# Performance work log

Hardware: AMD Instinct MI355X
Metric: run time of the kernel (lower is better)

## Reference

```python
import jax, jax.numpy as jnp
import numpy as np

C = 128        # attention channels (inner_channel)
OUT_C = 256    # bottleneck output channels (in_channel)
NEG = -10000000.0


def conv_bn_relu(x, W, scale, shift):
    """1x1 conv (no bias) + eval-mode BatchNorm folded to scale/shift + ReLU.
    x: [B, Cin, H, W], W: [Cout, Cin]."""
    y = jnp.einsum('oc,bchw->bohw', W, x)
    y = y * scale[None, :, None, None] + shift[None, :, None, None]
    return jax.nn.relu(y)


def setup_inputs() -> dict:
    key = jax.random.key(0)
    ks = jax.random.split(key, 20)
    B, H, W_, K = 4, 128, 128, 1024
    inp = {
        'query_feats': jax.random.normal(ks[0], (B, C, H, W_), jnp.float32),
        'key_feats':   jax.random.normal(ks[1], (B, C, K, 1), jnp.float32),
        'value_feats': jax.random.normal(ks[2], (B, C, K, 1), jnp.float32),
        'key_mask':    jax.random.randint(ks[3], (B, 1, K, 1), 0, 2).astype(bool),
    }
    s = 1.0 / np.sqrt(C)

    def mk(i, cin, cout):
        return (jax.random.normal(ks[i], (cout, cin), jnp.float32) * s,
                jnp.ones((cout,), jnp.float32),
                jnp.zeros((cout,), jnp.float32))

    inp['Wq1'], inp['sq1'], inp['bq1'] = mk(4, C, C)
    inp['Wq2'], inp['sq2'], inp['bq2'] = mk(5, C, C)
    inp['Wk1'], inp['sk1'], inp['bk1'] = mk(6, C, C)
    inp['Wk2'], inp['sk2'], inp['bk2'] = mk(7, C, C)
    inp['Wv'],  inp['sv'],  inp['bv']  = mk(8, C, C)
    inp['Wo'],  inp['so'],  inp['bo']  = mk(9, C, C)
    inp['Wb'],  inp['sb'],  inp['bb']  = mk(10, 2 * C, OUT_C)
    return inp


def reference(query_feats, key_feats, value_feats, key_mask,
              Wq1, sq1, bq1, Wq2, sq2, bq2,
              Wk1, sk1, bk1, Wk2, sk2, bk2,
              Wv, sv, bv, Wo, so, bo, Wb, sb, bb):
    B, _, H, W_ = query_feats.shape
    # projections (2 conv-bn-relu for q/k, 1 for v)
    q = conv_bn_relu(conv_bn_relu(query_feats, Wq1, sq1, bq1), Wq2, sq2, bq2)
    k = conv_bn_relu(conv_bn_relu(key_feats, Wk1, sk1, bk1), Wk2, sk2, bk2)
    v = conv_bn_relu(value_feats, Wv, sv, bv)

    q = q.reshape(B, C, -1).transpose(0, 2, 1)   # [B, HW, C]
    k = k.reshape(B, C, -1)                      # [B, C, K]
    v = v.reshape(B, C, -1).transpose(0, 2, 1)   # [B, K, C]

    sim = jnp.einsum('bqc,bck->bqk', q, k) * (C ** -0.5)   # [B, HW, K]
    m = key_mask.reshape(B, 1, -1).astype(sim.dtype)        # [B, 1, K]
    sim = sim * m + NEG * (1.0 - m)
    attn = jax.nn.softmax(sim, axis=-1)

    ctx = jnp.einsum('bqk,bkc->bqc', attn, v)               # [B, HW, C]
    ctx = ctx.transpose(0, 2, 1).reshape(B, C, H, W_)
    ctx = conv_bn_relu(ctx, Wo, so, bo)                     # out_project

    out = conv_bn_relu(jnp.concatenate([ctx, query_feats], axis=1), Wb, sb, bb)
    return out
```

## Files before the change

### kernel.cpp

```cpp
#include <hip/hip_runtime.h>
#include <hip/hip_bf16.h>

#define B_    4
#define C_    128
#define HW_   16384
#define K_    1024
#define NEG_  (-10000000.0f)
#define SCALE_ 0.08838834764831845f

using bf16 = __hip_bfloat16;
typedef __bf16 b8v __attribute__((ext_vector_type(8)));
typedef __bf16 b4v __attribute__((ext_vector_type(4)));
typedef __bf16 b2v __attribute__((ext_vector_type(2)));
typedef float  f4v __attribute__((ext_vector_type(4)));

__device__ __forceinline__ b8v ldb8(const void* p) { return *(const b8v*)p; }
__device__ __forceinline__ b4v ldb4(const void* p) { return *(const b4v*)p; }

#define XSTRIDE 272
#define KSTRIDE 272
#define VSTRIDE 136

__global__ __launch_bounds__(256) void prep1_kernel(
    const float* __restrict__ query, const float* __restrict__ key, const float* __restrict__ val,
    const float* __restrict__ Wq1, const float* __restrict__ sq1,
    const float* __restrict__ Wq2, const float* __restrict__ sq2,
    const float* __restrict__ Wo,  const float* __restrict__ so,
    const float* __restrict__ Wb,  const float* __restrict__ sb,
    const float* __restrict__ Wk1, const float* __restrict__ sk1,
    const float* __restrict__ Wk2, const float* __restrict__ sk2,
    const float* __restrict__ Wv,  const float* __restrict__ sv,
    bf16* __restrict__ qt, bf16* __restrict__ kT, bf16* __restrict__ vT,
    __bf16* __restrict__ Wq1p, __bf16* __restrict__ Wq2p,
    __bf16* __restrict__ Wop,  __bf16* __restrict__ Wbp,
    __bf16* __restrict__ Wk1p, __bf16* __restrict__ Wk2p, __bf16* __restrict__ Wvp)
{
    __shared__ float Xs[64 * 129];
    const int blk = blockIdx.x, t = threadIdx.x;

    if (blk < 1152) {
        const float* src; bf16* dst; int L, p0, b;
        if (blk < 1024) {
            b = blk >> 8; src = query; dst = qt; L = HW_; p0 = (blk & 255) * 64;
        } else {
            const int i = blk - 1024;
            b = i >> 5; int j = i & 31;
            if (j < 16) { src = key; dst = kT; } else { src = val; dst = vT; j -= 16; }
            L = K_; p0 = j * 64;
        }
        const int pl = t & 63, cg = t >> 6;
#pragma unroll 4
        for (int i = 0; i < 32; ++i) {
            const int c = cg * 32 + i;
            Xs[pl * 129 + c] = src[(size_t)(b * 128 + c) * L + p0 + pl];
        }
        __syncthreads();
#pragma unroll 4
        for (int it = 0; it < 16; ++it) {
            const int p = it * 4 + cg;
            b2v pk;
            pk[0] = (__bf16)Xs[p * 129 + 2 * pl];
            pk[1] = (__bf16)Xs[p * 129 + 2 * pl + 1];
            *(b2v*)(dst + ((size_t)b * L + p0 + p) * 128 + 2 * pl) = pk;
        }
    } else {
        const int idx = (blk - 1152) * 256 + t;
        if (idx < 16384)       { Wq1p[idx] = (__bf16)(Wq1[idx] * sq1[idx >> 7]); }
        else if (idx < 32768)  { const int i = idx - 16384;  Wq2p[i] = (__bf16)(Wq2[i] * sq2[i >> 7]); }
        else if (idx < 49152)  { const int i = idx - 32768;  Wop[i]  = (__bf16)(Wo[i]  * so[i >> 7]); }
        else if (idx < 114688) { const int i = idx - 49152;  Wbp[i]  = (__bf16)(Wb[i]  * sb[i >> 8]); }
        else if (idx < 131072) { const int i = idx - 114688; Wk1p[i] = (__bf16)(Wk1[i] * sk1[i >> 7]); }
        else if (idx < 147456) { const int i = idx - 131072; Wk2p[i] = (__bf16)(Wk2[i] * sk2[i >> 7]); }
        else                   { const int i = idx - 147456; Wvp[i]  = (__bf16)(Wv[i]  * sv[i >> 7]); }
    }
}

__device__ __forceinline__ void proj2_body(
    const bf16* __restrict__ src,
    const __bf16* __restrict__ W1, const float* __restrict__ sh1,
    const __bf16* __restrict__ W2, const float* __restrict__ sh2,
    bf16* __restrict__ dst, char* Xs, __bf16* Ys)
{
    const int t = threadIdx.x, w = t >> 6, lane = t & 63;
    const int pl = lane & 15, quad = lane >> 4;
    const int ob = 32 * w;

    {
        const char* sg = (const char*)src + t * 16;
        char* xl = Xs + (t >> 4) * XSTRIDE + (t & 15) * 16;
#pragma unroll
        for (int i = 0; i < 8; ++i)
            *(float4*)(xl + i * 16 * XSTRIDE) = *(const float4*)(sg + i * 4096);
    }

    b8v W1f[2][4], W2f[2][4];
#pragma unroll
    for (int mt = 0; mt < 2; ++mt)
#pragma unroll
        for (int s = 0; s < 4; ++s) {
            W1f[mt][s] = ldb8(W1 + (ob + mt * 16 + pl) * 128 + s * 32 + quad * 8);
            W2f[mt][s] = ldb8(W2 + (ob + mt * 16 + pl) * 128 + s * 32 + quad * 8);
        }
    __syncthreads();

    f4v acc[2][8];
#pragma unroll
    for (int mt = 0; mt < 2; ++mt)
#pragma unroll
        for (int nt = 0; nt < 8; ++nt) acc[mt][nt] = (f4v){0.f, 0.f, 0.f, 0.f};

#pragma unroll
    for (int s = 0; s < 4; ++s) {
        b8v Bf[8];
#pragma unroll
        for (int nt = 0; nt < 8; ++nt)
            Bf[nt] = ldb8(Xs + (nt * 16 + pl) * XSTRIDE + s * 64 + quad * 16);
#pragma unroll
        for (int mt = 0; mt < 2; ++mt)
#pragma unroll
            for (int nt = 0; nt < 8; ++nt)
                acc[mt][nt] = __builtin_amdgcn_mfma_f32_16x16x32_bf16(W1f[mt][s], Bf[nt], acc[mt][nt], 0, 0, 0);
    }

#pragma unroll
    for (int mt = 0; mt < 2; ++mt) {
        const float4 s4 = *(const float4*)(sh1 + ob + mt * 16 + quad * 4);
        const float shf[4] = {s4.x, s4.y, s4.z, s4.w};
#pragma unroll
        for (int nt = 0; nt < 8; ++nt) {
            b4v y;
#pragma unroll
            for (int r = 0; r < 4; ++r) y[r] = (__bf16)fmaxf(acc[mt][nt][r] + shf[r], 0.f);
            *(b4v*)&Ys[(nt * 16 + pl) * 136 + ob + mt * 16 + quad * 4] = y;
        }
    }
    __syncthreads();

    f4v acc2[2][8];
#pragma unroll
    for (int mt = 0; mt < 2; ++mt)
#pragma unroll
        for (int nt = 0; nt < 8; ++nt) acc2[mt][nt] = (f4v){0.f, 0.f, 0.f, 0.f};

#pragma unroll
    for (int s = 0; s < 4; ++s) {
        b8v Bf[8];
#pragma unroll
        for (int nt = 0; nt < 8; ++nt)
            Bf[nt] = *(const b8v*)&Ys[(nt * 16 + pl) * 136 + s * 32 + quad * 8];
#pragma unroll
        for (int mt = 0; mt < 2; ++mt)
#pragma unroll
            for (int nt = 0; nt < 8; ++nt)
                acc2[mt][nt] = __builtin_amdgcn_mfma_f32_16x16x32_bf16(W2f[mt][s], Bf[nt], acc2[mt][nt], 0, 0, 0);
    }

#pragma unroll
    for (int mt = 0; mt < 2; ++mt) {
        const float4 s4 = *(const float4*)(sh2 + ob + mt * 16 + quad * 4);
        const float shf[4] = {s4.x, s4.y, s4.z, s4.w};
#pragma unroll
        for (int nt = 0; nt < 8; ++nt) {
            b4v y;
#pragma unroll
            for (int r = 0; r < 4; ++r) y[r] = (__bf16)fmaxf(acc2[mt][nt][r] + shf[r], 0.f);
            *(b4v*)(dst + (size_t)(nt * 16 + pl) * 128 + ob + mt * 16 + quad * 4) = y;
        }
    }
}

__global__ __launch_bounds__(256, 2) void kvproj_kernel(
    const bf16* __restrict__ kT, const bf16* __restrict__ vT,
    const __bf16* __restrict__ Wk1p, const float* __restrict__ bk1,
    const __bf16* __restrict__ Wk2p, const float* __restrict__ bk2,
    const __bf16* __restrict__ Wvp,  const float* __restrict__ bv,
    bf16* __restrict__ kbuf, bf16* __restrict__ vbuf)
{
    __shared__ __align__(16) char Xs[128 * XSTRIDE];
    __shared__ __align__(16) __bf16 Ys[128 * 136];
    const int t = threadIdx.x, w = t >> 6, lane = t & 63;
    const int pl = lane & 15, quad = lane >> 4;
    const int b = blockIdx.y;
    const int n0 = blockIdx.x * 128;

    proj2_body(kT + ((size_t)b * K_ + n0) * 128, Wk1p, bk1, Wk2p, bk2,
               kbuf + ((size_t)b * K_ + n0) * 128, Xs, Ys);
    __syncthreads();

    {
        const char* sg = (const char*)(vT + ((size_t)b * K_ + n0) * 128) + t * 16;
        char* xl = Xs + (t >> 4) * XSTRIDE + (t & 15) * 16;
#pragma unroll
        for (int i = 0; i < 8; ++i)
            *(float4*)(xl + i * 16 * XSTRIDE) = *(const float4*)(sg + i * 4096);
    }
    const int ob = 32 * w;
    b8v Wf[2][4];
#pragma unroll
    for (int mt = 0; mt < 2; ++mt)
#pragma unroll
        for (int s = 0; s < 4; ++s)
            Wf[mt][s] = ldb8(Wvp + (ob + mt * 16 + pl) * 128 + s * 32 + quad * 8);
    __syncthreads();

    f4v acc[2][8];
#pragma unroll
    for (int mt = 0; mt < 2; ++mt)
#pragma unroll
        for (int nt = 0; nt < 8; ++nt) acc[mt][nt] = (f4v){0.f, 0.f, 0.f, 0.f};

#pragma unroll
    for (int s = 0; s < 4; ++s) {
        b8v Bf[8];
#pragma unroll
        for (int nt = 0; nt < 8; ++nt)
            Bf[nt] = ldb8(Xs + (nt * 16 + pl) * XSTRIDE + s * 64 + quad * 16);
#pragma unroll
        for (int mt = 0; mt < 2; ++mt)
#pragma unroll
            for (int nt = 0; nt < 8; ++nt)
                acc[mt][nt] = __builtin_amdgcn_mfma_f32_16x16x32_bf16(Wf[mt][s], Bf[nt], acc[mt][nt], 0, 0, 0);
    }

    bf16* vb = vbuf + (size_t)b * 128 * K_;
#pragma unroll
    for (int mt = 0; mt < 2; ++mt) {
        const float4 s4 = *(const float4*)(bv + ob + mt * 16 + quad * 4);
        const float shf[4] = {s4.x, s4.y, s4.z, s4.w};
#pragma unroll
        for (int nt = 0; nt < 8; ++nt)
#pragma unroll
            for (int r = 0; r < 4; ++r)
                vb[(size_t)(ob + mt * 16 + quad * 4 + r) * K_ + n0 + nt * 16 + pl]
                    = __float2bfloat16(fmaxf(acc[mt][nt][r] + shf[r], 0.f));
    }
}

__global__ __launch_bounds__(256, 2) void mega_kernel(
    const bf16* __restrict__ qt, const bf16* __restrict__ kbuf, const bf16* __restrict__ vbuf,
    const int* __restrict__ mask,
    const __bf16* __restrict__ Wq1p, const float* __restrict__ bq1,
    const __bf16* __restrict__ Wq2p, const float* __restrict__ bq2,
    const __bf16* __restrict__ Wop,  const float* __restrict__ bo,
    const __bf16* __restrict__ Wbp,  const float* __restrict__ bb,
    float* __restrict__ out)
{
    __shared__ __align__(16) char RA[128 * XSTRIDE];
    __shared__ __align__(16) char RB[128 * XSTRIDE];

    const int t = threadIdx.x, w = t >> 6, lane = t & 63;
    const int pl = lane & 15, quad = lane >> 4;
    const int n0 = blockIdx.x * 128;
    const int b  = blockIdx.y;
    const int ob = 32 * w;

    __bf16* RAh = (__bf16*)RA;
    __bf16* RBh = (__bf16*)RB;
    char* xl = RA + (t >> 4) * XSTRIDE + (t & 15) * 16;

    {
        const char* qg = (const char*)(qt + ((size_t)b * HW_ + n0) * 128) + t * 16;
#pragma unroll
        for (int i = 0; i < 8; ++i)
            *(float4*)(xl + i * 16 * XSTRIDE) = *(const float4*)(qg + i * 4096);
    }
    {
        b8v W1f[2][4], W2f[2][4];
#pragma unroll
        for (int mt = 0; mt < 2; ++mt)
#pragma unroll
            for (int s = 0; s < 4; ++s) {
                W1f[mt][s] = ldb8(Wq1p + (ob + mt * 16 + pl) * 128 + s * 32 + quad * 8);
                W2f[mt][s] = ldb8(Wq2p + (ob + mt * 16 + pl) * 128 + s * 32 + quad * 8);
            }
        __syncthreads();

        f4v a1[2][8];
#pragma unroll
        for (int mt = 0; mt < 2; ++mt)
#pragma unroll
            for (int nt = 0; nt < 8; ++nt) a1[mt][nt] = (f4v){0.f, 0.f, 0.f, 0.f};
#pragma unroll
        for (int s = 0; s < 4; ++s) {
            b8v Bf[8];
#pragma unroll
            for (int nt = 0; nt < 8; ++nt)
                Bf[nt] = ldb8(RA + (nt * 16 + pl) * XSTRIDE + s * 64 + quad * 16);
#pragma unroll
            for (int mt = 0; mt < 2; ++mt)
#pragma unroll
                for (int nt = 0; nt < 8; ++nt)
                    a1[mt][nt] = __builtin_amdgcn_mfma_f32_16x16x32_bf16(W1f[mt][s], Bf[nt], a1[mt][nt], 0, 0, 0);
        }
#pragma unroll
        for (int mt = 0; mt < 2; ++mt) {
            const float4 s4 = *(const float4*)(bq1 + ob + mt * 16 + quad * 4);
            const float shf[4] = {s4.x, s4.y, s4.z, s4.w};
#pragma unroll
            for (int nt = 0; nt < 8; ++nt) {
                b4v y;
#pragma unroll
                for (int r = 0; r < 4; ++r) y[r] = (__bf16)fmaxf(a1[mt][nt][r] + shf[r], 0.f);
                *(b4v*)&RBh[(nt * 16 + pl) * 136 + ob + mt * 16 + quad * 4] = y;
            }
        }
        __syncthreads();

        f4v a2[2][8];
#pragma unroll
        for (int mt = 0; mt < 2; ++mt)
#pragma unroll
            for (int nt = 0; nt < 8; ++nt) a2[mt][nt] = (f4v){0.f, 0.f, 0.f, 0.f};
#pragma unroll
        for (int s = 0; s < 4; ++s) {
            b8v Bf[8];
#pragma unroll
            for (int nt = 0; nt < 8; ++nt)
                Bf[nt] = *(const b8v*)&RBh[(nt * 16 + pl) * 136 + s * 32 + quad * 8];
#pragma unroll
            for (int mt = 0; mt < 2; ++mt)
#pragma unroll
                for (int nt = 0; nt < 8; ++nt)
                    a2[mt][nt] = __builtin_amdgcn_mfma_f32_16x16x32_bf16(W2f[mt][s], Bf[nt], a2[mt][nt], 0, 0, 0);
        }
#pragma unroll
        for (int mt = 0; mt < 2; ++mt) {
            const float4 s4 = *(const float4*)(bq2 + ob + mt * 16 + quad * 4);
            const float shf[4] = {s4.x, s4.y, s4.z, s4.w};
#pragma unroll
            for (int nt = 0; nt < 8; ++nt) {
                b4v y;
#pragma unroll
                for (int r = 0; r < 4; ++r) y[r] = (__bf16)fmaxf(a2[mt][nt][r] + shf[r], 0.f);
                *(b4v*)&RAh[(nt * 16 + pl) * 136 + ob + mt * 16 + quad * 4] = y;
            }
        }
        __syncthreads();
    }

    b8v qf0[4], qf1[4];
#pragma unroll
    for (int s = 0; s < 4; ++s) {
        qf0[s] = ldb8(RA + (w * 32 + pl) * XSTRIDE + s * 64 + quad * 16);
        qf1[s] = ldb8(RA + (w * 32 + 16 + pl) * XSTRIDE + s * 64 + quad * 16);
    }
    __syncthreads();

    float* bias = (float*)RA;
    char* ktile = RA + 4096;
    char* vtile = RB;

    for (int i = t; i < K_; i += 256)
        bias[i] = (mask[b * K_ + i] != 0) ? 0.f : NEG_;

    const bf16* kpt = kbuf + (size_t)b * K_ * 128;
    const bf16* vpt = vbuf + (size_t)b * 128 * K_;
    const char* kg = (const char*)kpt + t * 16;
    const char* vg = (const char*)(vpt + (size_t)(t >> 3) * K_) + (t & 7) * 16;
    char* kl = ktile + (t >> 4) * KSTRIDE + (t & 15) * 16;
    char* vl = vtile + (t >> 3) * VSTRIDE + (t & 7) * 16;

    float4 k_r0 = *(const float4*)(kg);
    float4 k_r1 = *(const float4*)(kg + 4096);
    float4 k_r2 = *(const float4*)(kg + 8192);
    float4 k_r3 = *(const float4*)(kg + 12288);
    float4 v_r0 = *(const float4*)(vg);
    float4 v_r1 = *(const float4*)(vg + 65536);
    float4 v_r2 = *(const float4*)(vg + 131072);
    float4 v_r3 = *(const float4*)(vg + 196608);

    f4v ac0[8], ac1[8];
#pragma unroll
    for (int i = 0; i < 8; ++i) { ac0[i] = (f4v){0.f,0.f,0.f,0.f}; ac1[i] = (f4v){0.f,0.f,0.f,0.f}; }
    float mrun0 = -3.0e38f, mrun1 = -3.0e38f, lrun0 = 0.f, lrun1 = 0.f;

    for (int chunk = 0; chunk < 16; ++chunk) {
        const int k0 = chunk * 64;

        *(float4*)(kl)                = k_r0;
        *(float4*)(kl + 16 * KSTRIDE) = k_r1;
        *(float4*)(kl + 32 * KSTRIDE) = k_r2;
        *(float4*)(kl + 48 * KSTRIDE) = k_r3;
        *(float4*)(vl)                = v_r0;
        *(float4*)(vl + 32 * VSTRIDE) = v_r1;
        *(float4*)(vl + 64 * VSTRIDE) = v_r2;
        *(float4*)(vl + 96 * VSTRIDE) = v_r3;
        __syncthreads();

        if (chunk < 15) {
            const char* kgn = kg + (chunk + 1) * 16384;
            const char* vgn = vg + (chunk + 1) * 128;
            k_r0 = *(const float4*)(kgn);
            k_r1 = *(const float4*)(kgn + 4096);
            k_r2 = *(const float4*)(kgn + 8192);
            k_r3 = *(const float4*)(kgn + 12288);
            v_r0 = *(const float4*)(vgn);
            v_r1 = *(const float4*)(vgn + 65536);
            v_r2 = *(const float4*)(vgn + 131072);
            v_r3 = *(const float4*)(vgn + 196608);
        }

        f4v sv0[4], sv1[4];
#pragma unroll
        for (int kt = 0; kt < 4; ++kt) {
            f4v a0 = (f4v){0.f,0.f,0.f,0.f}, a1 = (f4v){0.f,0.f,0.f,0.f};
            const char* krow = ktile + (kt * 16 + pl) * KSTRIDE + quad * 16;
#pragma unroll
            for (int s = 0; s < 4; ++s) {
                const b8v kf = ldb8(krow + s * 64);
                a0 = __builtin_amdgcn_mfma_f32_16x16x32_bf16(kf, qf0[s], a0, 0, 0, 0);
                a1 = __builtin_amdgcn_mfma_f32_16x16x32_bf16(kf, qf1[s], a1, 0, 0, 0);
            }
            const float4 b4 = *(const float4*)&bias[k0 + kt * 16 + quad * 4];
            const float bb4[4] = {b4.x, b4.y, b4.z, b4.w};
#pragma unroll
            for (int r = 0; r < 4; ++r) { sv0[kt][r] = a0[r] * SCALE_ + bb4[r];
                                          sv1[kt][r] = a1[r] * SCALE_ + bb4[r]; }
        }

        float ml0 = sv0[0][0], ml1 = sv1[0][0];
#pragma unroll
        for (int kt = 0; kt < 4; ++kt)
#pragma unroll
            for (int r = 0; r < 4; ++r) { ml0 = fmaxf(ml0, sv0[kt][r]); ml1 = fmaxf(ml1, sv1[kt][r]); }
        ml0 = fmaxf(ml0, __shfl_xor(ml0, 16, 64)); ml0 = fmaxf(ml0, __shfl_xor(ml0, 32, 64));
        ml1 = fmaxf(ml1, __shfl_xor(ml1, 16, 64)); ml1 = fmaxf(ml1, __shfl_xor(ml1, 32, 64));
        const float mn0 = fmaxf(mrun0, ml0), mn1 = fmaxf(mrun1, ml1);
        const float al0 = __expf(mrun0 - mn0), al1 = __expf(mrun1 - mn1);
        mrun0 = mn0; mrun1 = mn1;

        b4v pk0[4], pk1[4];
        float rs0 = 0.f, rs1 = 0.f;
#pragma unroll
        for (int kt = 0; kt < 4; ++kt)
#pragma unroll
            for (int r = 0; r < 4; ++r) {
                const float p0 = __expf(sv0[kt][r] - mn0); rs0 += p0; pk0[kt][r] = (__bf16)p0;
                const float p1 = __expf(sv1[kt][r] - mn1); rs1 += p1; pk1[kt][r] = (__bf16)p1;
            }
        rs0 += __shfl_xor(rs0, 16, 64); rs0 += __shfl_xor(rs0, 32, 64);
        rs1 += __shfl_xor(rs1, 16, 64); rs1 += __shfl_xor(rs1, 32, 64);
        lrun0 = lrun0 * al0 + rs0;
        lrun1 = lrun1 * al1 + rs1;

        float ar0[4], ar1[4];
#pragma unroll
        for (int r = 0; r < 4; ++r) { ar0[r] = __shfl(al0, quad * 4 + r, 64);
                                      ar1[r] = __shfl(al1, quad * 4 + r, 64); }
#pragma unroll
        for (int ct = 0; ct < 8; ++ct)
#pragma unroll
            for (int r = 0; r < 4; ++r) { ac0[ct][r] *= ar0[r]; ac1[ct][r] *= ar1[r]; }

        const b8v A00 = __builtin_shufflevector(pk0[0], pk0[1], 0, 1, 2, 3, 4, 5, 6, 7);
        const b8v A01 = __builtin_shufflevector(pk0[2], pk0[3], 0, 1, 2, 3, 4, 5, 6, 7);
        const b8v A10 = __builtin_shufflevector(pk1[0], pk1[1], 0, 1, 2, 3, 4, 5, 6, 7);
        const b8v A11 = __builtin_shufflevector(pk1[2], pk1[3], 0, 1, 2, 3, 4, 5, 6, 7);
#pragma unroll
        for (int ct = 0; ct < 8; ++ct) {
            const char* vrow = vtile + (ct * 16 + pl) * VSTRIDE + quad * 8;
            const b8v B0 = __builtin_shufflevector(ldb4(vrow),      ldb4(vrow + 32), 0, 1, 2, 3, 4, 5, 6, 7);
            const b8v B1 = __builtin_shufflevector(ldb4(vrow + 64), ldb4(vrow + 96), 0, 1, 2, 3, 4, 5, 6, 7);
            ac0[ct] = __builtin_amdgcn_mfma_f32_16x16x32_bf16(A00, B0, ac0[ct], 0, 0, 0);
            ac0[ct] = __builtin_amdgcn_mfma_f32_16x16x32_bf16(A01, B1, ac0[ct], 0, 0, 0);
            ac1[ct] = __builtin_amdgcn_mfma_f32_16x16x32_bf16(A10, B0, ac1[ct], 0, 0, 0);
            ac1[ct] = __builtin_amdgcn_mfma_f32_16x16x32_bf16(A11, B1, ac1[ct], 0, 0, 0);
        }
        __syncthreads();
    }

    {
        float inv0[4], inv1[4];
#pragma unroll
        for (int r = 0; r < 4; ++r) { inv0[r] = 1.f / __shfl(lrun0, quad * 4 + r, 64);
                                      inv1[r] = 1.f / __shfl(lrun1, quad * 4 + r, 64); }
#pragma unroll
        for (int ct = 0; ct < 8; ++ct)
#pragma unroll
            for (int r = 0; r < 4; ++r) {
                RAh[(w * 32 + quad * 4 + r) * 136 + ct * 16 + pl]      = (__bf16)(ac0[ct][r] * inv0[r]);
                RAh[(w * 32 + 16 + quad * 4 + r) * 136 + ct * 16 + pl] = (__bf16)(ac1[ct][r] * inv1[r]);
            }
    }
    __syncthreads();

    b8v Wof[2][4];
#pragma unroll
    for (int mt = 0; mt < 2; ++mt)
#pragma unroll
        for (int s = 0; s < 4; ++s)
            Wof[mt][s] = ldb8(Wop + (ob + mt * 16 + pl) * 128 + s * 32 + quad * 8);

    const char* qg2 = (const char*)(qt + ((size_t)b * HW_ + n0) * 128) + t * 16;
    float4 q_s0 = *(const float4*)(qg2);
    float4 q_s1 = *(const float4*)(qg2 + 4096);
    float4 q_s2 = *(const float4*)(qg2 + 8192);
    float4 q_s3 = *(const float4*)(qg2 + 12288);
    float4 q_s4 = *(const float4*)(qg2 + 16384);
    float4 q_s5 = *(const float4*)(qg2 + 20480);
    float4 q_s6 = *(const float4*)(qg2 + 24576);
    float4 q_s7 = *(const float4*)(qg2 + 28672);

    {
        f4v f1[2][8];
#pragma unroll
        for (int mt = 0; mt < 2; ++mt)
#pragma unroll
            for (int nt = 0; nt < 8; ++nt) f1[mt][nt] = (f4v){0.f, 0.f, 0.f, 0.f};
#pragma unroll
        for (int s = 0; s < 4; ++s) {
            b8v Bf[8];
#pragma unroll
            for (int nt = 0; nt < 8; ++nt)
                Bf[nt] = ldb8(RA + (nt * 16 + pl) * XSTRIDE + s * 64 + quad * 16);
#pragma unroll
            for (int mt = 0; mt < 2; ++mt)
#pragma unroll
                for (int nt = 0; nt < 8; ++nt)
                    f1[mt][nt] = __builtin_amdgcn_mfma_f32_16x16x32_bf16(Wof[mt][s], Bf[nt], f1[mt][nt], 0, 0, 0);
        }
#pragma unroll
        for (int mt = 0; mt < 2; ++mt) {
// ... 30 lines not shown
        for (int ks = 0; ks < 8; ++ks) {
            b8v Af[4];
#pragma unroll
            for (int mt = 0; mt < 4; ++mt)
                Af[mt] = ldb8(Wbp + (size_t)(64 * w + mt * 16 + pl) * 256 + ks * 32 + quad * 8);
            b8v Bf[8];
            if (ks < 4) {
#pragma unroll
                for (int nt = 0; nt < 8; ++nt)
                    Bf[nt] = *(const b8v*)&RBh[(nt * 16 + pl) * 136 + ks * 32 + quad * 8];
            } else {
#pragma unroll
                for (int nt = 0; nt < 8; ++nt)
                    Bf[nt] = ldb8(RA + (nt * 16 + pl) * XSTRIDE + (ks - 4) * 64 + quad * 16);
            }
#pragma unroll
            for (int mt = 0; mt < 4; ++mt)
#pragma unroll
                for (int nt = 0; nt < 8; ++nt)
                    f2[mt][nt] = __builtin_amdgcn_mfma_f32_16x16x32_bf16(Af[mt], Bf[nt], f2[mt][nt], 0, 0, 0);
        }
#pragma unroll
        for (int mt = 0; mt < 4; ++mt) {
            const float4 s4 = *(const float4*)(bb + 64 * w + mt * 16 + quad * 4);
            const float shf[4] = {s4.x, s4.y, s4.z, s4.w};
#pragma unroll
            for (int nt = 0; nt < 8; ++nt)
#pragma unroll
                for (int r = 0; r < 4; ++r)
                    out[(size_t)(b * 256 + 64 * w + mt * 16 + quad * 4 + r) * HW_ + n0 + nt * 16 + pl]
                        = fmaxf(f2[mt][nt][r] + shf[r], 0.f);
        }
    }
}

extern "C" void kernel_launch(void* const* d_in, const int* in_sizes, int n_in,
                              void* d_out, int out_size, void* d_ws, size_t ws_size,
                              hipStream_t stream)
{
    const float* query = (const float*)d_in[0];
    const float* key   = (const float*)d_in[1];
    const float* val   = (const float*)d_in[2];
    const int*   mask  = (const int*)  d_in[3];
    const float* Wq1 = (const float*)d_in[4];  const float* sq1 = (const float*)d_in[5];  const float* bq1 = (const float*)d_in[6];
    const float* Wq2 = (const float*)d_in[7];  const float* sq2 = (const float*)d_in[8];  const float* bq2 = (const float*)d_in[9];
    const float* Wk1 = (const float*)d_in[10]; const float* sk1 = (const float*)d_in[11]; const float* bk1 = (const float*)d_in[12];
    const float* Wk2 = (const float*)d_in[13]; const float* sk2 = (const float*)d_in[14]; const float* bk2 = (const float*)d_in[15];
    const float* Wv  = (const float*)d_in[16]; const float* sv  = (const float*)d_in[17]; const float* bv  = (const float*)d_in[18];
    const float* Wo  = (const float*)d_in[19]; const float* so  = (const float*)d_in[20]; const float* bo  = (const float*)d_in[21];
    const float* Wb  = (const float*)d_in[22]; const float* sb  = (const float*)d_in[23]; const float* bb  = (const float*)d_in[24];

    char* ws = (char*)d_ws;
    bf16*   qt   = (bf16*)(ws);
    bf16*   kT   = (bf16*)(ws + (16u << 20));
    bf16*   vT   = (bf16*)(ws + (17u << 20));
    bf16*   kbuf = (bf16*)(ws + (18u << 20));
    bf16*   vbuf = (bf16*)(ws + (19u << 20));
    char*   wbase = ws + (20u << 20);
    __bf16* Wq1p = (__bf16*)(wbase);
    __bf16* Wq2p = (__bf16*)(wbase + (32u << 10));
    __bf16* Wop  = (__bf16*)(wbase + (64u << 10));
    __bf16* Wbp  = (__bf16*)(wbase + (96u << 10));
    __bf16* Wk1p = (__bf16*)(wbase + (224u << 10));
    __bf16* Wk2p = (__bf16*)(wbase + (256u << 10));
    __bf16* Wvp  = (__bf16*)(wbase + (288u << 10));
    float* outp = (float*)d_out;

    prep1_kernel<<<1792, 256, 0, stream>>>(
        query, key, val,
        Wq1, sq1, Wq2, sq2, Wo, so, Wb, sb, Wk1, sk1, Wk2, sk2, Wv, sv,
        qt, kT, vT, Wq1p, Wq2p, Wop, Wbp, Wk1p, Wk2p, Wvp);
    kvproj_kernel<<<dim3(8, B_), 256, 0, stream>>>(
        kT, vT, Wk1p, bk1, Wk2p, bk2, Wvp, bv, kbuf, vbuf);
    mega_kernel<<<dim3(HW_ / 128, B_), 256, 0, stream>>>(
        qt, kbuf, vbuf, mask,
        Wq1p, bq1, Wq2p, bq2, Wop, bo, Wbp, bb, outp);
}
```

Measured before the change: 222.4 us.

## Fuse K/V projection into prep, double-buffer attention tiles, lazy softmax rescale

Moves the key/value projections into the prep kernel so the separate kvproj launch and the kT/vT intermediate buffers go away. Inside the mega kernel, K/V tiles are now double-buffered with loads issued two chunks ahead, and raw s_barrier plus setprio hints replace __syncthreads. The softmax switches to exp2 with the log2e factor folded into the scale and mask bias. The accumulator rescale is skipped unless the running max grows by more than a threshold. The V tile layout changes to allow wider LDS reads, at the cost of more LDS and register pressure. The lazy rescale can let exponentials reach up to 2^8 before correction, which narrows the numerical margin.

After: 231.7 us. 1.04x slower.

```diff
diff --git a/kernel.cpp b/kernel.cpp
--- a/kernel.cpp
+++ b/kernel.cpp
@@ -5,8 +5,9 @@
 #define C_    128
 #define HW_   16384
 #define K_    1024
-#define NEG_  (-10000000.0f)
-#define SCALE_ 0.08838834764831845f
+#define SC2_  0.12751734f
+#define NEGL_ (-1.4427e7f)
+#define DTHR_ 8.0f
 
 using bf16 = __hip_bfloat16;
 typedef __bf16 b8v __attribute__((ext_vector_type(8)));
@@ -15,224 +16,211 @@
 typedef float  f4v __attribute__((ext_vector_type(4)));
 
 __device__ __forceinline__ b8v ldb8(const void* p) { return *(const b8v*)p; }
-__device__ __forceinline__ b4v ldb4(const void* p) { return *(const b4v*)p; }
 
 #define XSTRIDE 272
 #define KSTRIDE 272
-#define VSTRIDE 136
-
-__global__ __launch_bounds__(256) void prep1_kernel(
+#define VSTRIDE 144
+
+__device__ __forceinline__ b8v ldw8(const float* wp, float sc) {
+    const float4 a = *(const float4*)wp;
+    const float4 c = *(const float4*)(wp + 4);
+    b8v r;
+    r[0] = (__bf16)(a.x * sc); r[1] = (__bf16)(a.y * sc);
+    r[2] = (__bf16)(a.z * sc); r[3] = (__bf16)(a.w * sc);
+    r[4] = (__bf16)(c.x * sc); r[5] = (__bf16)(c.y * sc);
+    r[6] = (__bf16)(c.z * sc); r[7] = (__bf16)(c.w * sc);
+    return r;
+}
+
+__global__ __launch_bounds__(256, 2) void prep_kernel(
     const float* __restrict__ query, const float* __restrict__ key, const float* __restrict__ val,
     const float* __restrict__ Wq1, const float* __restrict__ sq1,
     const float* __restrict__ Wq2, const float* __restrict__ sq2,
     const float* __restrict__ Wo,  const float* __restrict__ so,
     const float* __restrict__ Wb,  const float* __restrict__ sb,
-    const float* __restrict__ Wk1, const float* __restrict__ sk1,
-    const float* __restrict__ Wk2, const float* __restrict__ sk2,
-    const float* __restrict__ Wv,  const float* __restrict__ sv,
-    bf16* __restrict__ qt, bf16* __restrict__ kT, bf16* __restrict__ vT,
+    const float* __restrict__ Wk1, const float* __restrict__ sk1, const float* __restrict__ bk1,
+    const float* __restrict__ Wk2, const float* __restrict__ sk2, const float* __restrict__ bk2,
+    const float* __restrict__ Wv,  const float* __restrict__ sv_, const float* __restrict__ bv,
+    bf16* __restrict__ qt, bf16* __restrict__ kbuf, bf16* __restrict__ vbuf,
     __bf16* __restrict__ Wq1p, __bf16* __restrict__ Wq2p,
-    __bf16* __restrict__ Wop,  __bf16* __restrict__ Wbp,
-    __bf16* __restrict__ Wk1p, __bf16* __restrict__ Wk2p, __bf16* __restrict__ Wvp)
+    __bf16* __restrict__ Wop,  __bf16* __restrict__ Wbp)
 {
-    __shared__ float Xs[64 * 129];
+    __shared__ __align__(16) char SM[69632];
     const int blk = blockIdx.x, t = threadIdx.x;
 
-    if (blk < 1152) {
-        const float* src; bf16* dst; int L, p0, b;
-        if (blk < 1024) {
-            b = blk >> 8; src = query; dst = qt; L = HW_; p0 = (blk & 255) * 64;
-        } else {
-            const int i = blk - 1024;
-            b = i >> 5; int j = i & 31;
-            if (j < 16) { src = key; dst = kT; } else { src = val; dst = vT; j -= 16; }
-            L = K_; p0 = j * 64;
-        }
+    if (blk < 32) {
+        const int b = blk >> 3, n0 = (blk & 7) * 128;
+        const int w = t >> 6, lane = t & 63;
+        const int pl = lane & 15, quad = lane >> 4;
+        const int ob = 32 * w;
+        const int plT = t & 63, cg = t >> 6;
+        char*    Xs  = SM;
+        __bf16*  Ys  = (__bf16*)(SM + 34816);
+        float*   Tmp = (float*)(SM + 34816);
+
+        auto transpose_in = [&](const float* src) {
+#pragma unroll
+            for (int h = 0; h < 2; ++h) {
+                const int p0 = n0 + h * 64;
+#pragma unroll 4
+                for (int i2 = 0; i2 < 32; ++i2) {
+                    const int c = cg * 32 + i2;
+                    Tmp[plT * 129 + c] = src[(size_t)(b * 128 + c) * K_ + p0 + plT];
+                }
+                __syncthreads();
+#pragma unroll 4
+                for (int it = 0; it < 16; ++it) {
+                    const int p = it * 4 + cg;
+                    b2v pk2;
+                    pk2[0] = (__bf16)Tmp[p * 129 + 2 * plT];
+                    pk2[1] = (__bf16)Tmp[p * 129 + 2 * plT + 1];
+                    *(b2v*)(Xs + (h * 64 + p) * XSTRIDE + 4 * plT) = pk2;
+                }
+                __syncthreads();
+            }
+        };
+
+        transpose_in(key);
+        b8v W1f[2][4], W2f[2][4];
+#pragma unroll
+        for (int mt = 0; mt < 2; ++mt)
+#pragma unroll
+            for (int s = 0; s < 4; ++s) {
+                const int row = ob + mt * 16 + pl;
+                W1f[mt][s] = ldw8(Wk1 + row * 128 + s * 32 + quad * 8, sk1[row]);
+                W2f[mt][s] = ldw8(Wk2 + row * 128 + s * 32 + quad * 8, sk2[row]);
+            }
+        {
+            f4v acc[2][8];
+#pragma unroll
+            for (int mt = 0; mt < 2; ++mt)
+#pragma unroll
+                for (int nt = 0; nt < 8; ++nt) acc[mt][nt] = (f4v){0.f, 0.f, 0.f, 0.f};
+#pragma unroll
+            for (int s = 0; s < 4; ++s) {
+                b8v Bf[8];
+#pragma unroll
+                for (int nt = 0; nt < 8; ++nt)
+                    Bf[nt] = ldb8(Xs + (nt * 16 + pl) * XSTRIDE + s * 64 + quad * 16);
+#pragma unroll
+                for (int mt = 0; mt < 2; ++mt)
+#pragma unroll
+                    for (int nt = 0; nt < 8; ++nt)
+                        acc[mt][nt] = __builtin_amdgcn_mfma_f32_16x16x32_bf16(W1f[mt][s], Bf[nt], acc[mt][nt], 0, 0, 0);
+            }
+#pragma unroll
+            for (int mt = 0; mt < 2; ++mt) {
+                const float4 s4 = *(const float4*)(bk1 + ob + mt * 16 + quad * 4);
+                const float shf[4] = {s4.x, s4.y, s4.z, s4.w};
+#pragma unroll
+                for (int nt = 0; nt < 8; ++nt) {
+                    b4v y;
+#pragma unroll
+                    for (int r = 0; r < 4; ++r) y[r] = (__bf16)fmaxf(acc[mt][nt][r] + shf[r], 0.f);
+                    *(b4v*)&Ys[(nt * 16 + pl) * 136 + ob + mt * 16 + quad * 4] = y;
+                }
+            }
+        }
+        __syncthreads();
+        {
+            f4v acc2[2][8];
+#pragma unroll
+            for (int mt = 0; mt < 2; ++mt)
+#pragma unroll
+                for (int nt = 0; nt < 8; ++nt) acc2[mt][nt] = (f4v){0.f, 0.f, 0.f, 0.f};
+#pragma unroll
+            for (int s = 0; s < 4; ++s) {
+                b8v Bf[8];
+#pragma unroll
+                for (int nt = 0; nt < 8; ++nt)
+                    Bf[nt] = *(const b8v*)&Ys[(nt * 16 + pl) * 136 + s * 32 + quad * 8];
+#pragma unroll
+                for (int mt = 0; mt < 2; ++mt)
+#pragma unroll
+                    for (int nt = 0; nt < 8; ++nt)
+                        acc2[mt][nt] = __builtin_amdgcn_mfma_f32_16x16x32_bf16(W2f[mt][s], Bf[nt], acc2[mt][nt], 0, 0, 0);
+            }
+            bf16* kdst = kbuf + ((size_t)b * K_ + n0) * 128;
+#pragma unroll
+            for (int mt = 0; mt < 2; ++mt) {
+                const float4 s4 = *(const float4*)(bk2 + ob + mt * 16 + quad * 4);
+                const float shf[4] = {s4.x, s4.y, s4.z, s4.w};
+#pragma unroll
+                for (int nt = 0; nt < 8; ++nt) {
+                    b4v y;
+#pragma unroll
+                    for (int r = 0; r < 4; ++r) y[r] = (__bf16)fmaxf(acc2[mt][nt][r] + shf[r], 0.f);
+                    *(b4v*)(kdst + (size_t)(nt * 16 + pl) * 128 + ob + mt * 16 + quad * 4) = y;
+                }
+            }
+        }
+        __syncthreads();
+
+        transpose_in(val);
+        b8v Wvf[2][4];
+#pragma unroll
+        for (int mt = 0; mt < 2; ++mt)
+#pragma unroll
+            for (int s = 0; s < 4; ++s) {
+                const int row = ob + mt * 16 + pl;
+                Wvf[mt][s] = ldw8(Wv + row * 128 + s * 32 + quad * 8, sv_[row]);
+            }
+        {
+            f4v acc[2][8];
+#pragma unroll
+            for (int mt = 0; mt < 2; ++mt)
+#pragma unroll
+                for (int nt = 0; nt < 8; ++nt) acc[mt][nt] = (f4v){0.f, 0.f, 0.f, 0.f};
+#pragma unroll
+            for (int s = 0; s < 4; ++s) {
+                b8v Bf[8];
+#pragma unroll
+                for (int nt = 0; nt < 8; ++nt)
+                    Bf[nt] = ldb8(Xs + (nt * 16 + pl) * XSTRIDE + s * 64 + quad * 16);
+#pragma unroll
+                for (int mt = 0; mt < 2; ++mt)
+#pragma unroll
+                    for (int nt = 0; nt < 8; ++nt)
+                        acc[mt][nt] = __builtin_amdgcn_mfma_f32_16x16x32_bf16(Wvf[mt][s], Bf[nt], acc[mt][nt], 0, 0, 0);
+            }
+            bf16* vdst = vbuf + (size_t)b * 128 * K_;
+#pragma unroll
+            for (int mt = 0; mt < 2; ++mt) {
+                const float4 s4 = *(const float4*)(bv + ob + mt * 16 + quad * 4);
+                const float shf[4] = {s4.x, s4.y, s4.z, s4.w};
+#pragma unroll
+                for (int nt = 0; nt < 8; ++nt)
+#pragma unroll
+                    for (int r = 0; r < 4; ++r)
+                        vdst[(size_t)(ob + mt * 16 + quad * 4 + r) * K_ + n0 + nt * 16 + pl]
+                            = __float2bfloat16(fmaxf(acc[mt][nt][r] + shf[r], 0.f));
+            }
+        }
+    } else if (blk < 1056) {
+        float* Xs2 = (float*)SM;
+        const int i = blk - 32;
+        const int b = i >> 8, p0 = (i & 255) * 64;
         const int pl = t & 63, cg = t >> 6;
 #pragma unroll 4
-        for (int i = 0; i < 32; ++i) {
-            const int c = cg * 32 + i;
-            Xs[pl * 129 + c] = src[(size_t)(b * 128 + c) * L + p0 + pl];
+        for (int i2 = 0; i2 < 32; ++i2) {
+            const int c = cg * 32 + i2;
+            Xs2[pl * 129 + c] = query[(size_t)(b * 128 + c) * HW_ + p0 + pl];
         }
         __syncthreads();
 #pragma unroll 4
         for (int it = 0; it < 16; ++it) {
             const int p = it * 4 + cg;
-            b2v pk;
-            pk[0] = (__bf16)Xs[p * 129 + 2 * pl];
-            pk[1] = (__bf16)Xs[p * 129 + 2 * pl + 1];
-            *(b2v*)(dst + ((size_t)b * L + p0 + p) * 128 + 2 * pl) = pk;
+            b2v pk2;
+            pk2[0] = (__bf16)Xs2[p * 129 + 2 * pl];
+            pk2[1] = (__bf16)Xs2[p * 129 + 2 * pl + 1];
+            *(b2v*)(qt + ((size_t)b * HW_ + p0 + p) * 128 + 2 * pl) = pk2;
         }
     } else {
-        const int idx = (blk - 1152) * 256 + t;
-        if (idx < 16384)       { Wq1p[idx] = (__bf16)(Wq1[idx] * sq1[idx >> 7]); }
-        else if (idx < 32768)  { const int i = idx - 16384;  Wq2p[i] = (__bf16)(Wq2[i] * sq2[i >> 7]); }
-        else if (idx < 49152)  { const int i = idx - 32768;  Wop[i]  = (__bf16)(Wo[i]  * so[i >> 7]); }
-        else if (idx < 114688) { const int i = idx - 49152;  Wbp[i]  = (__bf16)(Wb[i]  * sb[i >> 8]); }
-        else if (idx < 131072) { const int i = idx - 114688; Wk1p[i] = (__bf16)(Wk1[i] * sk1[i >> 7]); }
-        else if (idx < 147456) { const int i = idx - 131072; Wk2p[i] = (__bf16)(Wk2[i] * sk2[i >> 7]); }
-        else                   { const int i = idx - 147456; Wvp[i]  = (__bf16)(Wv[i]  * sv[i >> 7]); }
-    }
-}
-
-__device__ __forceinline__ void proj2_body(
-    const bf16* __restrict__ src,
-    const __bf16* __restrict__ W1, const float* __restrict__ sh1,
-    const __bf16* __restrict__ W2, const float* __restrict__ sh2,
-    bf16* __restrict__ dst, char* Xs, __bf16* Ys)
-{
-    const int t = threadIdx.x, w = t >> 6, lane = t & 63;
-    const int pl = lane & 15, quad = lane >> 4;
-    const int ob = 32 * w;
-
-    {
-        const char* sg = (const char*)src + t * 16;
-        char* xl = Xs + (t >> 4) * XSTRIDE + (t & 15) * 16;
-#pragma unroll
-        for (int i = 0; i < 8; ++i)
-            *(float4*)(xl + i * 16 * XSTRIDE) = *(const float4*)(sg + i * 4096);
-    }
-
-    b8v W1f[2][4], W2f[2][4];
-#pragma unroll
-    for (int mt = 0; mt < 2; ++mt)
-#pragma unroll
-        for (int s = 0; s < 4; ++s) {
-            W1f[mt][s] = ldb8(W1 + (ob + mt * 16 + pl) * 128 + s * 32 + quad * 8);
-            W2f[mt][s] = ldb8(W2 + (ob + mt * 16 + pl) * 128 + s * 32 + quad * 8);
-        }
-    __syncthreads();
-
-    f4v acc[2][8];
-#pragma unroll
-    for (int mt = 0; mt < 2; ++mt)
-#pragma unroll
-        for (int nt = 0; nt < 8; ++nt) acc[mt][nt] = (f4v){0.f, 0.f, 0.f, 0.f};
-
-#pragma unroll
-    for (int s = 0; s < 4; ++s) {
-        b8v Bf[8];
-#pragma unroll
-        for (int nt = 0; nt < 8; ++nt)
-            Bf[nt] = ldb8(Xs + (nt * 16 + pl) * XSTRIDE + s * 64 + quad * 16);
-#pragma unroll
-        for (int mt = 0; mt < 2; ++mt)
-#pragma unroll
-            for (int nt = 0; nt < 8; ++nt)
-                acc[mt][nt] = __builtin_amdgcn_mfma_f32_16x16x32_bf16(W1f[mt][s], Bf[nt], acc[mt][nt], 0, 0, 0);
-    }
-
-#pragma unroll
-    for (int mt = 0; mt < 2; ++mt) {
-        const float4 s4 = *(const float4*)(sh1 + ob + mt * 16 + quad * 4);
-        const float shf[4] = {s4.x, s4.y, s4.z, s4.w};
-#pragma unroll
-        for (int nt = 0; nt < 8; ++nt) {
-            b4v y;
-#pragma unroll
-            for (int r = 0; r < 4; ++r) y[r] = (__bf16)fmaxf(acc[mt][nt][r] + shf[r], 0.f);
-            *(b4v*)&Ys[(nt * 16 + pl) * 136 + ob + mt * 16 + quad * 4] = y;
-        }
-    }
-    __syncthreads();
-
-    f4v acc2[2][8];
-#pragma unroll
-    for (int mt = 0; mt < 2; ++mt)
-#pragma unroll
-        for (int nt = 0; nt < 8; ++nt) acc2[mt][nt] = (f4v){0.f, 0.f, 0.f, 0.f};
-
-#pragma unroll
-    for (int s = 0; s < 4; ++s) {
-        b8v Bf[8];
-#pragma unroll
-        for (int nt = 0; nt < 8; ++nt)
-            Bf[nt] = *(const b8v*)&Ys[(nt * 16 + pl) * 136 + s * 32 + quad * 8];
-#pragma unroll
-        for (int mt = 0; mt < 2; ++mt)
-#pragma unroll
-            for (int nt = 0; nt < 8; ++nt)
-                acc2[mt][nt] = __builtin_amdgcn_mfma_f32_16x16x32_bf16(W2f[mt][s], Bf[nt], acc2[mt][nt], 0, 0, 0);
-    }
-
-#pragma unroll
-    for (int mt = 0; mt < 2; ++mt) {
-        const float4 s4 = *(const float4*)(sh2 + ob + mt * 16 + quad * 4);
-        const float shf[4] = {s4.x, s4.y, s4.z, s4.w};
-#pragma unroll
-        for (int nt = 0; nt < 8; ++nt) {
-            b4v y;
-#pragma unroll
-            for (int r = 0; r < 4; ++r) y[r] = (__bf16)fmaxf(acc2[mt][nt][r] + shf[r], 0.f);
-            *(b4v*)(dst + (size_t)(nt * 16 + pl) * 128 + ob + mt * 16 + quad * 4) = y;
-        }
-    }
-}
-
-__global__ __launch_bounds__(256, 2) void kvproj_kernel(
-    const bf16* __restrict__ kT, const bf16* __restrict__ vT,
-    const __bf16* __restrict__ Wk1p, const float* __restrict__ bk1,
-    const __bf16* __restrict__ Wk2p, const float* __restrict__ bk2,
-    const __bf16* __restrict__ Wvp,  const float* __restrict__ bv,
-    bf16* __restrict__ kbuf, bf16* __restrict__ vbuf)
-{
-    __shared__ __align__(16) char Xs[128 * XSTRIDE];
-    __shared__ __align__(16) __bf16 Ys[128 * 136];
-    const int t = threadIdx.x, w = t >> 6, lane = t & 63;
-    const int pl = lane & 15, quad = lane >> 4;
-    const int b = blockIdx.y;
-    const int n0 = blockIdx.x * 128;
-
-    proj2_body(kT + ((size_t)b * K_ + n0) * 128, Wk1p, bk1, Wk2p, bk2,
-               kbuf + ((size_t)b * K_ + n0) * 128, Xs, Ys);
-    __syncthreads();
-
-    {
-        const char* sg = (const char*)(vT + ((size_t)b * K_ + n0) * 128) + t * 16;
-        char* xl = Xs + (t >> 4) * XSTRIDE + (t & 15) * 16;
-#pragma unroll
-        for (int i = 0; i < 8; ++i)
-            *(float4*)(xl + i * 16 * XSTRIDE) = *(const float4*)(sg + i * 4096);
-    }
-    const int ob = 32 * w;
-    b8v Wf[2][4];
-#pragma unroll
-    for (int mt = 0; mt < 2; ++mt)
-#pragma unroll
-        for (int s = 0; s < 4; ++s)
-            Wf[mt][s] = ldb8(Wvp + (ob + mt * 16 + pl) * 128 + s * 32 + quad * 8);
-    __syncthreads();
-
-    f4v acc[2][8];
-#pragma unroll
-    for (int mt = 0; mt < 2; ++mt)
-#pragma unroll
-        for (int nt = 0; nt < 8; ++nt) acc[mt][nt] = (f4v){0.f, 0.f, 0.f, 0.f};
-
-#pragma unroll
-    for (int s = 0; s < 4; ++s) {
-        b8v Bf[8];
-#pragma unroll
-        for (int nt = 0; nt < 8; ++nt)
-            Bf[nt] = ldb8(Xs + (nt * 16 + pl) * XSTRIDE + s * 64 + quad * 16);
-#pragma unroll
-        for (int mt = 0; mt < 2; ++mt)
-#pragma unroll
-            for (int nt = 0; nt < 8; ++nt)
-                acc[mt][nt] = __builtin_amdgcn_mfma_f32_16x16x32_bf16(Wf[mt][s], Bf[nt], acc[mt][nt], 0, 0, 0);
-    }
-
-    bf16* vb = vbuf + (size_t)b * 128 * K_;
-#pragma unroll
-    for (int mt = 0; mt < 2; ++mt) {
-        const float4 s4 = *(const float4*)(bv + ob + mt * 16 + quad * 4);
-        const float shf[4] = {s4.x, s4.y, s4.z, s4.w};
-#pragma unroll
-        for (int nt = 0; nt < 8; ++nt)
-#pragma unroll
-            for (int r = 0; r < 4; ++r)
-                vb[(size_t)(ob + mt * 16 + quad * 4 + r) * K_ + n0 + nt * 16 + pl]
-                    = __float2bfloat16(fmaxf(acc[mt][nt][r] + shf[r], 0.f));
+        const int idx = (blk - 1056) * 256 + t;
+        if (idx < 16384)      { Wq1p[idx] = (__bf16)(Wq1[idx] * sq1[idx >> 7]); }
+        else if (idx < 32768) { const int i2 = idx - 16384; Wq2p[i2] = (__bf16)(Wq2[i2] * sq2[i2 >> 7]); }
+        else if (idx < 49152) { const int i2 = idx - 32768; Wop[i2]  = (__bf16)(Wo[i2]  * so[i2 >> 7]); }
+        else                  { const int i2 = idx - 49152; Wbp[i2]  = (__bf16)(Wb[i2]  * sb[i2 >> 8]); }
     }
 }
 
@@ -245,8 +233,7 @@
     const __bf16* __restrict__ Wbp,  const float* __restrict__ bb,
     float* __restrict__ out)
 {
-    __shared__ __align__(16) char RA[128 * XSTRIDE];
-    __shared__ __align__(16) char RB[128 * XSTRIDE];
+    __shared__ __align__(16) char S[75776];
 
     const int t = threadIdx.x, w = t >> 6, lane = t & 63;
     const int pl = lane & 15, quad = lane >> 4;
@@ -254,8 +241,9 @@
     const int b  = blockIdx.y;
     const int ob = 32 * w;
 
-    __bf16* RAh = (__bf16*)RA;
-    __bf16* RBh = (__bf16*)RB;
+    char*   RA  = S;
+    __bf16* RAh = (__bf16*)S;
+    __bf16* RBh = (__bf16*)(S + 34816);
     char* xl = RA + (t >> 4) * XSTRIDE + (t & 15) * 16;
 
     {
@@ -346,65 +334,81 @@
     }
     __syncthreads();
 
-    float* bias = (float*)RA;
-    char* ktile = RA + 4096;
-    char* vtile = RB;
-
-    for (int i = t; i < K_; i += 256)
-        bias[i] = (mask[b * K_ + i] != 0) ? 0.f : NEG_;
+    float* bias = (float*)S;
+    char* kt0 = S + 4096;
+    char* kt1 = S + 21504;
+    char* vt0 = S + 38912;
+    char* vt1 = S + 57344;
 
     const bf16* kpt = kbuf + (size_t)b * K_ * 128;
     const bf16* vpt = vbuf + (size_t)b * 128 * K_;
     const char* kg = (const char*)kpt + t * 16;
     const char* vg = (const char*)(vpt + (size_t)(t >> 3) * K_) + (t & 7) * 16;
-    char* kl = ktile + (t >> 4) * KSTRIDE + (t & 15) * 16;
-    char* vl = vtile + (t >> 3) * VSTRIDE + (t & 7) * 16;
-
-    float4 k_r0 = *(const float4*)(kg);
-    float4 k_r1 = *(const float4*)(kg + 4096);
-    float4 k_r2 = *(const float4*)(kg + 8192);
-    float4 k_r3 = *(const float4*)(kg + 12288);
-    float4 v_r0 = *(const float4*)(vg);
-    float4 v_r1 = *(const float4*)(vg + 65536);
-    float4 v_r2 = *(const float4*)(vg + 131072);
-    float4 v_r3 = *(const float4*)(vg + 196608);
+    const int klo = (t >> 4) * KSTRIDE + (t & 15) * 16;
+    const int vj  = t & 7;
+    const int vlo = (t >> 3) * VSTRIDE + (vj >> 2) * 64 + (vj & 1) * 32 + ((vj >> 1) & 1) * 8;
+
+    float4 kr[4], vr[4];
+
+#define ISSUE_LOADS(chunk)                                            \
+    { const char* kgn = kg + (chunk) * 16384;                         \
+      const char* vgn = vg + (chunk) * 128;                           \
+      kr[0] = *(const float4*)(kgn);                                  \
+      kr[1] = *(const float4*)(kgn + 4096);                           \
+      kr[2] = *(const float4*)(kgn + 8192);                           \
+      kr[3] = *(const float4*)(kgn + 12288);                          \
+      vr[0] = *(const float4*)(vgn);                                  \
+      vr[1] = *(const float4*)(vgn + 65536);                          \
+      vr[2] = *(const float4*)(vgn + 131072);                         \
+      vr[3] = *(const float4*)(vgn + 196608); }
+
+#define STAGE_WRITES(ktd, vtd)                                        \
+    { char* klp = (ktd) + klo;                                        \
+      *(float4*)(klp)                = kr[0];                         \
+      *(float4*)(klp + 16 * KSTRIDE) = kr[1];                         \
+      *(float4*)(klp + 32 * KSTRIDE) = kr[2];                         \
+      *(float4*)(klp + 48 * KSTRIDE) = kr[3];                         \
+      char* vlp = (vtd) + vlo;                                        \
+      *(float2*)(vlp)                     = make_float2(vr[0].x, vr[0].y); \
+      *(float2*)(vlp + 16)                = make_float2(vr[0].z, vr[0].w); \
+      *(float2*)(vlp + 32 * VSTRIDE)      = make_float2(vr[1].x, vr[1].y); \
+      *(float2*)(vlp + 32 * VSTRIDE + 16) = make_float2(vr[1].z, vr[1].w); \
+      *(float2*)(vlp + 64 * VSTRIDE)      = make_float2(vr[2].x, vr[2].y); \
+      *(float2*)(vlp + 64 * VSTRIDE + 16) = make_float2(vr[2].z, vr[2].w); \
+      *(float2*)(vlp + 96 * VSTRIDE)      = make_float2(vr[3].x, vr[3].y); \
+      *(float2*)(vlp + 96 * VSTRIDE + 16) = make_float2(vr[3].z, vr[3].w); }
+
+#define RAW_BARRIER()                                                 \
+    __builtin_amdgcn_sched_barrier(0);                                \
+    asm volatile("s_waitcnt lgkmcnt(0)" ::: "memory");                \
+    __builtin_amdgcn_s_barrier();                                     \
+    __builtin_amdgcn_sched_barrier(0);
+
+    ISSUE_LOADS(0)
+    for (int i2 = t; i2 < K_; i2 += 256)
+        bias[i2] = (mask[b * K_ + i2] != 0) ? 0.f : NEGL_;
+    STAGE_WRITES(kt0, vt0)
+    ISSUE_LOADS(1)
 
     f4v ac0[8], ac1[8];
 #pragma unroll
     for (int i = 0; i < 8; ++i) { ac0[i] = (f4v){0.f,0.f,0.f,0.f}; ac1[i] = (f4v){0.f,0.f,0.f,0.f}; }
     float mrun0 = -3.0e38f, mrun1 = -3.0e38f, lrun0 = 0.f, lrun1 = 0.f;
 
-    for (int chunk = 0; chunk < 16; ++chunk) {
-        const int k0 = chunk * 64;
-
-        *(float4*)(kl)                = k_r0;
-        *(float4*)(kl + 16 * KSTRIDE) = k_r1;
-        *(float4*)(kl + 32 * KSTRIDE) = k_r2;
-        *(float4*)(kl + 48 * KSTRIDE) = k_r3;
-        *(float4*)(vl)                = v_r0;
-        *(float4*)(vl + 32 * VSTRIDE) = v_r1;
-        *(float4*)(vl + 64 * VSTRIDE) = v_r2;
-        *(float4*)(vl + 96 * VSTRIDE) = v_r3;
-        __syncthreads();
-
-        if (chunk < 15) {
-            const char* kgn = kg + (chunk + 1) * 16384;
-            const char* vgn = vg + (chunk + 1) * 128;
-            k_r0 = *(const float4*)(kgn);
-            k_r1 = *(const float4*)(kgn + 4096);
-            k_r2 = *(const float4*)(kgn + 8192);
-            k_r3 = *(const float4*)(kgn + 12288);
-            v_r0 = *(const float4*)(vgn);
-            v_r1 = *(const float4*)(vgn + 65536);
-            v_r2 = *(const float4*)(vgn + 131072);
-            v_r3 = *(const float4*)(vgn + 196608);
-        }
+    RAW_BARRIER()
+
+#pragma unroll 2
+    for (int ch = 0; ch < 16; ++ch) {
+        const char* ktc = (ch & 1) ? kt1 : kt0;
+        const char* vtc = (ch & 1) ? vt1 : vt0;
+        const int k0 = ch * 64;
 
         f4v sv0[4], sv1[4];
+        __builtin_amdgcn_s_setprio(1);
 #pragma unroll
         for (int kt = 0; kt < 4; ++kt) {
             f4v a0 = (f4v){0.f,0.f,0.f,0.f}, a1 = (f4v){0.f,0.f,0.f,0.f};
-            const char* krow = ktile + (kt * 16 + pl) * KSTRIDE + quad * 16;
+            const char* krow = ktc + (kt * 16 + pl) * KSTRIDE + quad * 16;
 #pragma unroll
             for (int s = 0; s < 4; ++s) {
                 const b8v kf = ldb8(krow + s * 64);
@@ -414,8 +418,14 @@
             const float4 b4 = *(const float4*)&bias[k0 + kt * 16 + quad * 4];
             const float bb4[4] = {b4.x, b4.y, b4.z, b4.w};
 #pragma unroll
-            for (int r = 0; r < 4; ++r) { sv0[kt][r] = a0[r] * SCALE_ + bb4[r];
-                                          sv1[kt][r] = a1[r] * SCALE_ + bb4[r]; }
+            for (int r = 0; r < 4; ++r) { sv0[kt][r] = a0[r] * SC2_ + bb4[r];
+                                          sv1[kt][r] = a1[r] * SC2_ + bb4[r]; }
+        }
+        __builtin_amdgcn_s_setprio(0);
+
+        if (ch < 15) {
+            if (ch & 1) { STAGE_WRITES(kt0, vt0) } else { STAGE_WRITES(kt1, vt1) }
+            if (ch < 14) ISSUE_LOADS(ch + 2)
         }
 
         float ml0 = sv0[0][0], ml1 = sv1[0][0];
@@ -425,9 +435,21 @@
             for (int r = 0; r < 4; ++r) { ml0 = fmaxf(ml0, sv0[kt][r]); ml1 = fmaxf(ml1, sv1[kt][r]); }
         ml0 = fmaxf(ml0, __shfl_xor(ml0, 16, 64)); ml0 = fmaxf(ml0, __shfl_xor(ml0, 32, 64));
         ml1 = fmaxf(ml1, __shfl_xor(ml1, 16, 64)); ml1 = fmaxf(ml1, __shfl_xor(ml1, 32, 64));
-        const float mn0 = fmaxf(mrun0, ml0), mn1 = fmaxf(mrun1, ml1);
-        const float al0 = __expf(mrun0 - mn0), al1 = __expf(mrun1 - mn1);
-        mrun0 = mn0; mrun1 = mn1;
+
+        if (__any((ml0 > mrun0 + DTHR_) || (ml1 > mrun1 + DTHR_))) {
+            const float mn0 = fmaxf(mrun0, ml0), mn1 = fmaxf(mrun1, ml1);
+            const float al0 = exp2f(mrun0 - mn0), al1 = exp2f(mrun1 - mn1);
+            lrun0 *= al0; lrun1 *= al1;
+            mrun0 = mn0;  mrun1 = mn1;
+            float ar0[4], ar1[4];
+#pragma unroll
+            for (int r = 0; r < 4; ++r) { ar0[r] = __shfl(al0, quad * 4 + r, 64);
+                                          ar1[r] = __shfl(al1, quad * 4 + r, 64); }
+#pragma unroll
+            for (int ct = 0; ct < 8; ++ct)
+#pragma unroll
+                for (int r = 0; r < 4; ++r) { ac0[ct][r] *= ar0[r]; ac1[ct][r] *= ar1[r]; }
+        }
 
         b4v pk0[4], pk1[4];
         float rs0 = 0.f, rs1 = 0.f;
@@ -435,39 +457,35 @@
         for (int kt = 0; kt < 4; ++kt)
 #pragma unroll
             for (int r = 0; r < 4; ++r) {
-                const float p0 = __expf(sv0[kt][r] - mn0); rs0 += p0; pk0[kt][r] = (__bf16)p0;
-                const float p1 = __expf(sv1[kt][r] - mn1); rs1 += p1; pk1[kt][r] = (__bf16)p1;
+                const float p0 = exp2f(sv0[kt][r] - mrun0); rs0 += p0; pk0[kt][r] = (__bf16)p0;
+                const float p1 = exp2f(sv1[kt][r] - mrun1); rs1 += p1; pk1[kt][r] = (__bf16)p1;
             }
         rs0 += __shfl_xor(rs0, 16, 64); rs0 += __shfl_xor(rs0, 32, 64);
         rs1 += __shfl_xor(rs1, 16, 64); rs1 += __shfl_xor(rs1, 32, 64);
-        lrun0 = lrun0 * al0 + rs0;
-        lrun1 = lrun1 * al1 + rs1;
-
-        float ar0[4], ar1[4];
-#pragma unroll
-        for (int r = 0; r < 4; ++r) { ar0[r] = __shfl(al0, quad * 4 + r, 64);
-                                      ar1[r] = __shfl(al1, quad * 4 + r, 64); }
-#pragma unroll
-        for (int ct = 0; ct < 8; ++ct)
-#pragma unroll
-            for (int r = 0; r < 4; ++r) { ac0[ct][r] *= ar0[r]; ac1[ct][r] *= ar1[r]; }
+        lrun0 += rs0; lrun1 += rs1;
 
         const b8v A00 = __builtin_shufflevector(pk0[0], pk0[1], 0, 1, 2, 3, 4, 5, 6, 7);
         const b8v A01 = __builtin_shufflevector(pk0[2], pk0[3], 0, 1, 2, 3, 4, 5, 6, 7);
         const b8v A10 = __builtin_shufflevector(pk1[0], pk1[1], 0, 1, 2, 3, 4, 5, 6, 7);
         const b8v A11 = __builtin_shufflevector(pk1[2], pk1[3], 0, 1, 2, 3, 4, 5, 6, 7);
+        __builtin_amdgcn_s_setprio(1);
 #pragma unroll
         for (int ct = 0; ct < 8; ++ct) {
-            const char* vrow = vtile + (ct * 16 + pl) * VSTRIDE + quad * 8;
-            const b8v B0 = __builtin_shufflevector(ldb4(vrow),      ldb4(vrow + 32), 0, 1, 2, 3, 4, 5, 6, 7);
-            const b8v B1 = __builtin_shufflevector(ldb4(vrow + 64), ldb4(vrow + 96), 0, 1, 2, 3, 4, 5, 6, 7);
+            const char* vrow = vtc + (ct * 16 + pl) * VSTRIDE + quad * 16;
+            const b8v B0 = ldb8(vrow);
+            const b8v B1 = ldb8(vrow + 64);
             ac0[ct] = __builtin_amdgcn_mfma_f32_16x16x32_bf16(A00, B0, ac0[ct], 0, 0, 0);
             ac0[ct] = __builtin_amdgcn_mfma_f32_16x16x32_bf16(A01, B1, ac0[ct], 0, 0, 0);
             ac1[ct] = __builtin_amdgcn_mfma_f32_16x16x32_bf16(A10, B0, ac1[ct], 0, 0, 0);
             ac1[ct] = __builtin_amdgcn_mfma_f32_16x16x32_bf16(A11, B1, ac1[ct], 0, 0, 0);
         }
-        __syncthreads();
-    }
+        __builtin_amdgcn_s_setprio(0);
+
+        RAW_BARRIER()
+    }
+#undef ISSUE_LOADS
+#undef STAGE_WRITES
+#undef RAW_BARRIER
 
     {
         float inv0[4], inv1[4];
@@ -604,26 +622,20 @@
 
     char* ws = (char*)d_ws;
     bf16*   qt   = (bf16*)(ws);
-    bf16*   kT   = (bf16*)(ws + (16u << 20));
-    bf16*   vT   = (bf16*)(ws + (17u << 20));
-    bf16*   kbuf = (bf16*)(ws + (18u << 20));
-    bf16*   vbuf = (bf16*)(ws + (19u << 20));
-    char*   wbase = ws + (20u << 20);
+    bf16*   kbuf = (bf16*)(ws + (16u << 20));
+    bf16*   vbuf = (bf16*)(ws + (17u << 20));
+    char*   wbase = ws + (18u << 20);
     __bf16* Wq1p = (__bf16*)(wbase);
     __bf16* Wq2p = (__bf16*)(wbase + (32u << 10));
     __bf16* Wop  = (__bf16*)(wbase + (64u << 10));
     __bf16* Wbp  = (__bf16*)(wbase + (96u << 10));
-    __bf16* Wk1p = (__bf16*)(wbase + (224u << 10));
-    __bf16* Wk2p = (__bf16*)(wbase + (256u << 10));
-    __bf16* Wvp  = (__bf16*)(wbase + (288u << 10));
     float* outp = (float*)d_out;
 
-    prep1_kernel<<<1792, 256, 0, stream>>>(
+    prep_kernel<<<1504, 256, 0, stream>>>(
         query, key, val,
-        Wq1, sq1, Wq2, sq2, Wo, so, Wb, sb, Wk1, sk1, Wk2, sk2, Wv, sv,
-        qt, kT, vT, Wq1p, Wq2p, Wop, Wbp, Wk1p, Wk2p, Wvp);
-    kvproj_kernel<<<dim3(8, B_), 256, 0, stream>>>(
-        kT, vT, Wk1p, bk1, Wk2p, bk2, Wvp, bv, kbuf, vbuf);
+        Wq1, sq1, Wq2, sq2, Wo, so, Wb, sb,
+        Wk1, sk1, bk1, Wk2, sk2, bk2, Wv, sv, bv,
+        qt, kbuf, vbuf, Wq1p, Wq2p, Wop, Wbp);
     mega_kernel<<<dim3(HW_ / 128, B_), 256, 0, stream>>>(
         qt, kbuf, vbuf, mask,
         Wq1p, bq1, Wq2p, bq2, Wop, bo, Wbp, bb, outp);
```
